# Kernel optimization log

Hardware: AMD Instinct MI355X
Metric: run time of the kernel (lower is better)

## Reference

```python
import jax, jax.numpy as jnp
import numpy as np

N = 512            # hidden_state
BATCH = 64
L = 8192           # seq_len; kernel_max_size == L so kernel length = L
MIN_DELTA = 1e-3
MAX_DELTA = 0.1


def _hippo(n):
    idx = np.arange(n)
    init = np.sqrt(2.0 * idx + 1.0)
    H = np.outer(init, init)           # init @ init.T
    H = np.tril(H)                      # zero strict upper triangle
    H[idx, idx] -= idx                  # diag -= arange(N)
    return (-H).astype(np.float32)


def setup_inputs() -> dict:
    key = jax.random.key(0)
    kx, kb, kc, kd = jax.random.split(key, 4)
    X = jax.random.normal(kx, (BATCH, L), dtype=jnp.float32)
    A = jnp.asarray(_hippo(N))                                   # [N,N] HiPPO init
    Bm = jax.random.normal(kb, (N, 1), dtype=jnp.float32) * (1.0 / N) ** 0.5
    C = jax.random.normal(kc, (1, N), dtype=jnp.float32)
    D = jnp.ones((1,), dtype=jnp.float32)
    log_delta = jax.random.uniform(
        kd, (1,), dtype=jnp.float32,
        minval=np.log(MIN_DELTA), maxval=np.log(MAX_DELTA))
    return {"X": X, "A": A, "Bm": Bm, "C": C, "D": D, "log_delta": log_delta}


def reference(X, A, Bm, C, D, log_delta):
    # delta = exp(clamp(log_delta, log(min), log(max)))
    delta = jnp.exp(jnp.clip(log_delta, jnp.log(MIN_DELTA), jnp.log(MAX_DELTA)))[0]
    # bilinear (Tustin) discretization
    I = jnp.eye(N, dtype=X.dtype)
    A1 = I - delta * 0.5 * A
    A2 = I + delta * 0.5 * A
    Ad = jnp.linalg.solve(A1, A2)           # [N,N]
    Bd = jnp.linalg.solve(A1, delta * Bm)   # [N,1]

    # kernel k[t] = C @ Ad^t @ Bd, t = 0..L-1 (sequential scan)
    def step(v, _):
        return Ad @ v, (C @ v)[0, 0]
    _, k = jax.lax.scan(step, Bd, None, length=L)  # [L]

    # FFT linear (causal) convolution, truncated to L
    end = L + L - 1
    Xd = jnp.fft.rfft(X, n=end, axis=-1)      # [B, F]
    Kd = jnp.fft.rfft(k, n=end)               # [F]
    y = jnp.fft.irfft(Xd * Kd, n=end, axis=-1)[..., :L]
    return y + D * X
```

## Files before the change

kernel.cpp:

```cpp
#include <hip/hip_runtime.h>

#define N 512
#define L 8192

#define LOG_MIN -6.907755278982137f
#define LOG_MAX -2.302585092994046f

typedef __attribute__((ext_vector_type(8))) short short8;
typedef __attribute__((ext_vector_type(4))) float f32x4;

__device__ __forceinline__ float get_delta(const float* logd) {
  float ld = logd[0];
  ld = fminf(fmaxf(ld, LOG_MIN), LOG_MAX);
  return expf(ld);
}
__device__ __forceinline__ unsigned short f2bf(float x) {
  union { float f; unsigned int u; } c; c.f = x;
  unsigned int u = c.u;
  u += 0x7FFFu + ((u >> 16) & 1u);
  return (unsigned short)(u >> 16);
}
__device__ __forceinline__ unsigned int pack2(unsigned short a, unsigned short b) {
  return (unsigned int)a | ((unsigned int)b << 16);
}

__device__ __forceinline__ void ast(float* p, float v) {
  __hip_atomic_store(p, v, __ATOMIC_RELAXED, __HIP_MEMORY_SCOPE_AGENT);
}
__device__ __forceinline__ void ast4(float* p, float4 v) {
  ast(p, v.x); ast(p + 1, v.y); ast(p + 2, v.z); ast(p + 3, v.w);
}
__device__ __forceinline__ void astu(unsigned* p, unsigned v) {
  __hip_atomic_store(p, v, __ATOMIC_RELAXED, __HIP_MEMORY_SCOPE_AGENT);
}

__device__ __forceinline__ void gsync(unsigned* bar, int p, unsigned tgt) {
  asm volatile("s_waitcnt vmcnt(0)" ::: "memory");
  __syncthreads();
  if (threadIdx.x == 0) {
    __hip_atomic_fetch_add(&bar[p], 1u, __ATOMIC_RELAXED, __HIP_MEMORY_SCOPE_AGENT);
    while (__hip_atomic_load(&bar[p], __ATOMIC_RELAXED, __HIP_MEMORY_SCOPE_AGENT) < tgt)
      __builtin_amdgcn_s_sleep(2);
  }
  __syncthreads();
}


__device__ void diag64(const float* __restrict__ A, float h,
                       float* __restrict__ Xi, int blk, int tid, float* sm) {
  float* Ash = sm;
  float* xs  = sm + 4160;
  float* dinv = sm + 8320;
  int i0 = blk * 64;
  int r = tid >> 2, c0 = (tid & 3) * 16;
#pragma unroll
  for (int q = 0; q < 16; q += 4) {
    float4 v = *(const float4*)(A + (size_t)(i0 + r) * N + i0 + c0 + q);
    Ash[r * 65 + c0 + q] = v.x; Ash[r * 65 + c0 + q + 1] = v.y;
    Ash[r * 65 + c0 + q + 2] = v.z; Ash[r * 65 + c0 + q + 3] = v.w;
  }
  for (int i = tid; i < 4160; i += 256) xs[i] = 0.f;
  __syncthreads();
  if (tid < 64) dinv[tid] = 1.f / (1.f - h * Ash[tid * 65 + tid]);
  __syncthreads();
  int t = tid >> 2, sub = tid & 3;
  for (int rr = 0; rr < 64; ++rr) {
    if (t <= rr) {
      float s = 0.f;
      for (int k = t + sub; k < rr; k += 4) s += Ash[rr * 65 + k] * xs[k * 65 + t];
      s += __shfl_xor(s, 1, 64);
      s += __shfl_xor(s, 2, 64);
      if (sub == 0)
        xs[rr * 65 + t] = (((rr == t) ? 1.f : 0.f) + h * s) * dinv[rr];
    }
  }
  __syncthreads();
#pragma unroll
  for (int q = 0; q < 16; q += 4) {
    float4 v = {xs[r * 65 + c0 + q], xs[r * 65 + c0 + q + 1],
                xs[r * 65 + c0 + q + 2], xs[r * 65 + c0 + q + 3]};
    ast4(Xi + (size_t)(i0 + r) * N + i0 + c0 + q, v);
  }
}

template <int NT>
__device__ void gemm32t(const float* __restrict__ A_, int lda,
                        const float* __restrict__ B_, int ldb,
                        float* __restrict__ C_, int ldc,
                        int bi, int bj, float alpha, int tid, float* sm) {
  float* As = sm;
  float* Bs = sm + 1056;
  int tx = tid & 31, ty = tid >> 5;
  int lr = tid >> 3, lc = (tid & 7) * 4;
  const float* ap = A_ + (size_t)(bi * 32 + lr) * lda + lc;
  const float* bp = B_ + (size_t)lr * ldb + bj * 32 + lc;
  float4 aR[NT], bR[NT];
#pragma unroll
  for (int t = 0; t < NT; ++t) {
    aR[t] = *(const float4*)(ap + 32 * t);
    bR[t] = *(const float4*)(bp + (size_t)(32 * t) * ldb);
  }
  float acc[4] = {0.f, 0.f, 0.f, 0.f};
#pragma unroll
  for (int t = 0; t < NT; ++t) {
    As[lr * 33 + lc] = aR[t].x; As[lr * 33 + lc + 1] = aR[t].y;
    As[lr * 33 + lc + 2] = aR[t].z; As[lr * 33 + lc + 3] = aR[t].w;
    Bs[lr * 33 + lc] = bR[t].x; Bs[lr * 33 + lc + 1] = bR[t].y;
    Bs[lr * 33 + lc + 2] = bR[t].z; Bs[lr * 33 + lc + 3] = bR[t].w;
    __syncthreads();
#pragma unroll
    for (int kk = 0; kk < 32; ++kk) {
      float bv = Bs[kk * 33 + tx];
#pragma unroll
      for (int m = 0; m < 4; ++m) acc[m] += As[(ty + 8 * m) * 33 + kk] * bv;
    }
    __syncthreads();
  }
#pragma unroll
  for (int m = 0; m < 4; ++m)
    ast(&C_[(size_t)(bi * 32 + ty + 8 * m) * ldc + bj * 32 + tx], alpha * acc[m]);
}

__device__ void sq32(const float* __restrict__ P, float* __restrict__ Q,
                     int bi, int bj, int first, int tid, float* sm) {
  float* As = sm;
  float* Bs = sm + 1056;
  int tx = tid & 31, ty = tid >> 5;
  int lr = tid >> 3, lc = (tid & 7) * 4;
  int nk = bi - bj + 1;
  int kb0 = bj * 32;
  int arow = bi * 32 + lr;
  const float* ap = P + (size_t)arow * N + lc;
  const float* bp = P + bj * 32 + lc;
  float4 aR[16], bR[16];
#pragma unroll
  for (int t = 0; t < 16; ++t) {
    if (t < nk) {
      int kt = kb0 + 32 * t;
      aR[t] = *(const float4*)(ap + kt);
      bR[t] = *(const float4*)(bp + (size_t)(kt + lr) * N);
    }
  }
  float acc[4] = {0.f, 0.f, 0.f, 0.f};
#pragma unroll
  for (int t = 0; t < 16; ++t) {
    if (t < nk) {
      int kb = kb0 + 32 * t;
      float a4[4] = {aR[t].x, aR[t].y, aR[t].z, aR[t].w};
      float b4[4] = {bR[t].x, bR[t].y, bR[t].z, bR[t].w};
      if (first) {
#pragma unroll
        for (int j = 0; j < 4; ++j) {
          a4[j] = 2.f * a4[j] - ((arow == kb + lc + j) ? 1.f : 0.f);
          b4[j] = 2.f * b4[j] - ((kb + lr == bj * 32 + lc + j) ? 1.f : 0.f);
        }
      }
      As[lr * 33 + lc] = a4[0]; As[lr * 33 + lc + 1] = a4[1];
      As[lr * 33 + lc + 2] = a4[2]; As[lr * 33 + lc + 3] = a4[3];
      Bs[lr * 33 + lc] = b4[0]; Bs[lr * 33 + lc + 1] = b4[1];
      Bs[lr * 33 + lc + 2] = b4[2]; Bs[lr * 33 + lc + 3] = b4[3];
      __syncthreads();
#pragma unroll
      for (int kk = 0; kk < 32; ++kk) {
        float bv = Bs[kk * 33 + tx];
#pragma unroll
        for (int m = 0; m < 4; ++m) acc[m] += As[(ty + 8 * m) * 33 + kk] * bv;
      }
      __syncthreads();
    }
  }
#pragma unroll
  for (int m = 0; m < 4; ++m)
    ast(&Q[(size_t)(bi * 32 + ty + 8 * m) * N + bj * 32 + tx], acc[m]);
}

__device__ void vstep_g(const float* __restrict__ P, float* __restrict__ Vtr,
                        int base, int first, int idx, int tid, float* sm) {
  int bi = idx & 15, cj = idx >> 4;
  float* As = sm;
  float* Bs = sm + 1056;
  int tx = tid & 31, ty = tid >> 5;
  int lr = tid >> 3, lc = (tid & 7) * 4;
  int nrow = bi * 32 + lr;
  int crow = cj * 32 + lr;
  int cok = (crow < base);
  const float* ap = P + (size_t)nrow * N + lc;
  const float* bp = Vtr + (size_t)crow * N + lc;
  int nk = bi + 1;
  float4 aR[16], bR[16];
#pragma unroll
  for (int t = 0; t < 16; ++t) {
    if (t < nk) {
      aR[t] = *(const float4*)(ap + 32 * t);
      bR[t] = cok ? *(const float4*)(bp + 32 * t) : make_float4(0.f, 0.f, 0.f, 0.f);
    }
  }
  float acc[4] = {0.f, 0.f, 0.f, 0.f};
#pragma unroll
  for (int t = 0; t < 16; ++t) {
    if (t < nk) {
      int kb = 32 * t;
      float a4[4] = {aR[t].x, aR[t].y, aR[t].z, aR[t].w};
      if (first) {
#pragma unroll
        for (int j = 0; j < 4; ++j)
          a4[j] = 2.f * a4[j] - ((nrow == kb + lc + j) ? 1.f : 0.f);
      }
      As[lr * 33 + lc] = a4[0]; As[lr * 33 + lc + 1] = a4[1];
      As[lr * 33 + lc + 2] = a4[2]; As[lr * 33 + lc + 3] = a4[3];
      Bs[lr * 33 + lc] = bR[t].x; Bs[lr * 33 + lc + 1] = bR[t].y;
      Bs[lr * 33 + lc + 2] = bR[t].z; Bs[lr * 33 + lc + 3] = bR[t].w;
      __syncthreads();
#pragma unroll
      for (int kk = 0; kk < 32; ++kk) {
        float bv = Bs[tx * 33 + kk];
#pragma unroll
        for (int m = 0; m < 4; ++m) acc[m] += As[(ty + 8 * m) * 33 + kk] * bv;
      }
      __syncthreads();
    }
  }
  int c = cj * 32 + tx;
  if (c < base) {
#pragma unroll
    for (int m = 0; m < 4; ++m)
      ast(&Vtr[(size_t)(base + c) * N + bi * 32 + ty + 8 * m], acc[m]);
  }
}

__device__ void wstep_g(const float* __restrict__ P, float* __restrict__ W,
                        int base, int cj, int tid, float* sm) {
  float* As = sm;
  float* Bs = sm + 1056;
  int tx = tid & 31, ty = tid >> 5;
  int lr = tid >> 3, lc = (tid & 7) * 4;
  int qok = (lr < base);
  const float* ap = W + (size_t)lr * N + lc;
  const float* bp = P + cj * 32 + lc;
  int kb0 = cj * 32;
  int nk = 16 - cj;
  float4 aR[16], bR[16];
#pragma unroll
  for (int t = 0; t < 16; ++t) {
    if (t < nk) {
      int kt = kb0 + 32 * t;
      aR[t] = qok ? *(const float4*)(ap + kt) : make_float4(0.f, 0.f, 0.f, 0.f);
      bR[t] = *(const float4*)(bp + (size_t)(kt + lr) * N);
    }
  }
  float acc[4] = {0.f, 0.f, 0.f, 0.f};
#pragma unroll
  for (int t = 0; t < 16; ++t) {
    if (t < nk) {
      As[lr * 33 + lc] = aR[t].x; As[lr * 33 + lc + 1] = aR[t].y;
      As[lr * 33 + lc + 2] = aR[t].z; As[lr * 33 + lc + 3] = aR[t].w;
      Bs[lr * 33 + lc] = bR[t].x; Bs[lr * 33 + lc + 1] = bR[t].y;
      Bs[lr * 33 + lc + 2] = bR[t].z; Bs[lr * 33 + lc + 3] = bR[t].w;
      __syncthreads();
#pragma unroll
      for (int kk = 0; kk < 32; ++kk) {
        float bv = Bs[kk * 33 + tx];
#pragma unroll
        for (int m = 0; m < 4; ++m) acc[m] += As[(ty + 8 * m) * 33 + kk] * bv;
      }
      __syncthreads();
    }
  }
#pragma unroll
  for (int m = 0; m < 4; ++m) {
    int q = ty + 8 * m;
    if (q < base) ast(&W[(size_t)(base + q) * N + cj * 32 + tx], acc[m]);
  }
}

__device__ void kfinal_g(const float* __restrict__ W, const float* __restrict__ Vtr,
                         float* __restrict__ kvec, int bi, int bj, int tid, float* sm) {
  float* As = sm;
  float* Bs = sm + 1056;
  int tx = tid & 31, ty = tid >> 5;
  int lr = tid >> 3, lc = (tid & 7) * 4;
  const float* ap = W + (size_t)(bi * 32 + lr) * N + lc;
  const float* bp = Vtr + (size_t)(bj * 32 + lr) * N + lc;
  float4 aR[16], bR[16];
#pragma unroll
  for (int t = 0; t < 16; ++t) {
    aR[t] = *(const float4*)(ap + 32 * t);
    bR[t] = *(const float4*)(bp + 32 * t);
  }
  float acc[4] = {0.f, 0.f, 0.f, 0.f};
#pragma unroll
  for (int t = 0; t < 16; ++t) {
    As[lr * 33 + lc] = aR[t].x; As[lr * 33 + lc + 1] = aR[t].y;
    As[lr * 33 + lc + 2] = aR[t].z; As[lr * 33 + lc + 3] = aR[t].w;
    Bs[lr * 33 + lc] = bR[t].x; Bs[lr * 33 + lc + 1] = bR[t].y;
    Bs[lr * 33 + lc + 2] = bR[t].z; Bs[lr * 33 + lc + 3] = bR[t].w;
    __syncthreads();
#pragma unroll
    for (int kk = 0; kk < 32; ++kk) {
      float bv = Bs[tx * 33 + kk];
#pragma unroll
      for (int m = 0; m < 4; ++m) acc[m] += As[(ty + 8 * m) * 33 + kk] * bv;
    }
    __syncthreads();
  }
#pragma unroll
  for (int m = 0; m < 4; ++m)
    ast(&kvec[(size_t)(bi * 32 + ty + 8 * m) * 128 + bj * 32 + tx], acc[m]);
}

__device__ void bd1_body(const float* __restrict__ Xi, const float* __restrict__ Bm,
                         float delta, float* __restrict__ Vtr, int blk, int tid,
                         float* sm) {
  float* bs = sm;
  if (tid < 128) ((float4*)bs)[tid] = ((const float4*)Bm)[tid];
  __syncthreads();
  int w = tid >> 6, lane = tid & 63;
#pragma unroll
  for (int pass = 0; pass < 2; ++pass) {
    int row = blk * 8 + w * 2 + pass;
    const float* Xr = Xi + (size_t)row * N + lane * 8;
    float4 a0 = *(const float4*)Xr;
    float4 a1 = *(const float4*)(Xr + 4);
    const float* bp = bs + lane * 8;
    float acc = a0.x * bp[0] + a0.y * bp[1] + a0.z * bp[2] + a0.w * bp[3]
              + a1.x * bp[4] + a1.y * bp[5] + a1.z * bp[6] + a1.w * bp[7];
    acc += __shfl_xor(acc, 1, 64);
    acc += __shfl_xor(acc, 2, 64);
    acc += __shfl_xor(acc, 4, 64);
    acc += __shfl_xor(acc, 8, 64);
    acc += __shfl_xor(acc, 16, 64);
    acc += __shfl_xor(acc, 32, 64);
    if (lane == 0) ast(&Vtr[row], delta * acc);
  }
}

__device__ __forceinline__ void afrag_unit(const float* __restrict__ X,
                                           unsigned* __restrict__ Atab, int u) {
  int lane = u & 63;
  int f = u >> 6;
  int bt = f >> 8, ut = f & 255;
  int row = bt * 16 + (lane & 15);
  int u0 = ut * 32 + ((lane >> 4) << 3);
  const float* xp = X + (size_t)row * L + u0;
  unsigned short v[8];
#pragma unroll
  for (int e = 0; e < 8; ++e) v[e] = f2bf(xp[e]);
  unsigned* q = Atab + ((size_t)f * 64 + lane) * 4;
  astu(q, pack2(v[0], v[1])); astu(q + 1, pack2(v[2], v[3]));
  astu(q + 2, pack2(v[4], v[5])); astu(q + 3, pack2(v[6], v[7]));
}

__device__ __forceinline__ void bfrag_unit(const float* __restrict__ kvec,
                                           unsigned* __restrict__ Btab, int u) {
  int lane = u & 63;
  int si = u >> 6;
  int base = si * 16 + (lane & 15) - ((lane >> 4) << 3);
  unsigned short v[8];
#pragma unroll
  for (int e = 0; e < 8; ++e) {
    int idx = base - e;
    float x = (idx >= 0) ? kvec[idx] : 0.0f;
    v[e] = f2bf(x);
  }
  unsigned* q = Btab + ((size_t)si * 64 + lane) * 4;
  astu(q, pack2(v[0], v[1])); astu(q + 1, pack2(v[2], v[3]));
  astu(q + 2, pack2(v[4], v[5])); astu(q + 3, pack2(v[6], v[7]));
}

#define NB 168u

__global__ __launch_bounds__(256, 2) void k_chain(
    const float* __restrict__ A, const float* __restrict__ Bm,
    const float* __restrict__ C, const float* __restrict__ logd,
    const float* __restrict__ X,
    float* __restrict__ Xi, float* __restrict__ U1, float* __restrict__ U2,
    float* __restrict__ U3, float* __restrict__ PB,
    float* __restrict__ Vtr, float* __restrict__ W, float* __restrict__ kvec,
    unsigned* __restrict__ Atab, unsigned* __restrict__ Btab,
    unsigned* bar) {
  __shared__ float sm[8704];
  int b = blockIdx.x, tid = threadIdx.x;
  float delta = get_delta(logd);
  float h = 0.5f * delta;
#define PBUF(i) (PB + (size_t)(i) * (N * N))

  int sbi = 0, srem = b;
  while (srem > sbi) { srem -= (sbi + 1); ++sbi; }
  int sbj = srem;

  if (b < 8) {
    diag64(A, h, Xi, b, tid, sm);
  } else if (b < 36) {
    int idx = b - 8, bi = 0, bj = 0, cnt = 0;
    for (int i = 0; i < 8; ++i)
      for (int j = i + 1; j < 8; ++j) { if (cnt == idx) { bi = i; bj = j; } ++cnt; }
    int r = tid >> 2, c0 = (tid & 3) * 16;
    float4 z = {0.f, 0.f, 0.f, 0.f};
#pragma unroll
    for (int q = 0; q < 16; q += 4)
      ast4(Xi + (size_t)(bi * 64 + r) * N + bj * 64 + c0 + q, z);
  } else if (b == 36) {
    for (int i = tid; i < N; i += 256) ast(&W[i], C[i]);
  } else if (b >= 40) {
    int base = (b - 40) * 512;
    afrag_unit(X, Atab, base + tid);
    afrag_unit(X, Atab, base + 256 + tid);
  }
  gsync(bar, 0, NB);
  if (b < 16) {
    int g = b >> 2, t = b & 3;
    gemm32t<2>(A + (size_t)(128 * g + 64) * N + 128 * g, N,
               Xi + (size_t)(128 * g) * (N + 1), N,
               U1 + g * 4096, 64, t >> 1, t & 1, 1.0f, tid, sm);
  }
  gsync(bar, 1, NB);
  if (b < 16) {
    int g = b >> 2, t = b & 3;
    gemm32t<2>(Xi + (size_t)(128 * g + 64) * (N + 1), N, U1 + g * 4096, 64,
               Xi + (size_t)(128 * g + 64) * N + 128 * g, N, t >> 1, t & 1, h, tid, sm);
  }
  gsync(bar, 2, NB);
  if (b < 32) {
    int g = b >> 4, t = b & 15;
    gemm32t<4>(A + (size_t)(256 * g + 128) * N + 256 * g, N,
               Xi + (size_t)(256 * g) * (N + 1), N,
               U2 + g * 16384, 128, t >> 2, t & 3, 1.0f, tid, sm);
  }
  gsync(bar, 3, NB);
  if (b < 32) {
    int g = b >> 4, t = b & 15;
    gemm32t<4>(Xi + (size_t)(256 * g + 128) * (N + 1), N, U2 + g * 16384, 128,
               Xi + (size_t)(256 * g + 128) * N + 256 * g, N, t >> 2, t & 3, h, tid, sm);
  }
  gsync(bar, 4, NB);
  if (b < 64)
    gemm32t<8>(A + (size_t)256 * N, N, Xi, N, U3, 256, b >> 3, b & 7, 1.0f, tid, sm);
  gsync(bar, 5, NB);
  if (b < 64)
    gemm32t<8>(Xi + (size_t)256 * (N + 1), N, U3, 256,
               Xi + (size_t)256 * N, N, b >> 3, b & 7, h, tid, sm);
  gsync(bar, 6, NB);
  if (b < 64) bd1_body(Xi, Bm, delta, Vtr, b, tid, sm);
  gsync(bar, 7, NB);
  if (b < 136) sq32(Xi, PBUF(0), sbi, sbj, 1, tid, sm);
  else if (b < 152) vstep_g(Xi, Vtr, 1, 1, b - 136, tid, sm);
  gsync(bar, 8, NB);
  if (b < 136) sq32(PBUF(0), PBUF(1), sbi, sbj, 0, tid, sm);
  else if (b < 152) vstep_g(PBUF(0), Vtr, 2, 0, b - 136, tid, sm);
  gsync(bar, 9, NB);
  if (b < 136) sq32(PBUF(1), PBUF(2), sbi, sbj, 0, tid, sm);
  else if (b < 152) vstep_g(PBUF(1), Vtr, 4, 0, b - 136, tid, sm);
  gsync(bar, 10, NB);
  if (b < 136) sq32(PBUF(2), PBUF(3), sbi, sbj, 0, tid, sm);
  else if (b < 152) vstep_g(PBUF(2), Vtr, 8, 0, b - 136, tid, sm);
  gsync(bar, 11, NB);
  if (b < 136) sq32(PBUF(3), PBUF(4), sbi, sbj, 0, tid, sm);
  else if (b < 152) vstep_g(PBUF(3), Vtr, 16, 0, b - 136, tid, sm);
  gsync(bar, 12, NB);
  if (b < 136) sq32(PBUF(4), PBUF(5), sbi, sbj, 0, tid, sm);
  else if (b < 152) vstep_g(PBUF(4), Vtr, 32, 0, b - 136, tid, sm);
  gsync(bar, 13, NB);
  if (b < 136) sq32(PBUF(5), PBUF(6), sbi, sbj, 0, tid, sm);
  else vstep_g(PBUF(5), Vtr, 64, 0, b - 136, tid, sm);
  gsync(bar, 14, NB);
  if (b < 136) sq32(PBUF(6), PBUF(7), sbi, sbj, 0, tid, sm);
  else if (b < 152) wstep_g(PBUF(6), W, 1, b - 136, tid, sm);
  gsync(bar, 15, NB);
  if (b < 136) sq32(PBUF(7), PBUF(8), sbi, sbj, 0, tid, sm);
  else if (b < 152) wstep_g(PBUF(7), W, 2, b - 136, tid, sm);
  gsync(bar, 16, NB);
  if (b < 136) sq32(PBUF(8), PBUF(9), sbi, sbj, 0, tid, sm);
  else if (b < 152) wstep_g(PBUF(8), W, 4, b - 136, tid, sm);
  gsync(bar, 17, NB);
  if (b < 136) sq32(PBUF(9), PBUF(10), sbi, sbj, 0, tid, sm);
  else if (b < 152) wstep_g(PBUF(9), W, 8, b - 136, tid, sm);
  gsync(bar, 18, NB);
  if (b < 136) sq32(PBUF(10), PBUF(11), sbi, sbj, 0, tid, sm);
  else if (b < 152) wstep_g(PBUF(10), W, 16, b - 136, tid, sm);
  gsync(bar, 19, NB);
  if (b >= 136 && b < 152) wstep_g(PBUF(11), W, 32, b - 136, tid, sm);
  gsync(bar, 20, NB);
  if (b < 8) kfinal_g(W, Vtr, kvec, b >> 2, b & 3, tid, sm);
  gsync(bar, 21, NB);
  if (b < 128) bfrag_unit(kvec, Btab, b * 256 + tid);
#undef PBUF
}

__global__ __launch_bounds__(256, 2) void k_convmm(const short8* __restrict__ Atab,
                                                   const short8* __restrict__ Btab,
                                                   const float* __restrict__ X,
                                                   const float* __restrict__ Dp,
                                                   float* __restrict__ Y) {
  __shared__ short8 bsh[32][64];
  int tid = threadIdx.x, lane = tid & 63, bt = tid >> 6;
  int p = blockIdx.x;
  int jL = p, jH = 511 - p;
  int nL = (jL + 2) >> 1, nH = (jH + 2) >> 1;
  f32x4 aL = {0.f, 0.f, 0.f, 0.f}, aH = {0.f, 0.f, 0.f, 0.f};
  const short8* Abase = Atab + (size_t)bt * 256 * 64 + lane;
  for (int u0 = 0; u0 < nH; u0 += 16) {
#pragma unroll
    for (int k = 0; k < 8; ++k) {
      int idx = tid + 256 * k;
      int f = idx >> 6, ln = idx & 63;
      int i = f & 15;
      int ut = u0 + i;
      if (f < 16) {
        if (ut < nH) bsh[i][ln] = Btab[(size_t)(jH - 2 * ut) * 64 + ln];
      } else {
        if (ut < nL) bsh[16 + i][ln] = Btab[(size_t)(jL - 2 * ut) * 64 + ln];
      }
    }
    __syncthreads();
    int m = (nH - u0 < 16) ? (nH - u0) : 16;
    short8 a = Abase[(size_t)u0 * 64];
    for (int i = 0; i < m; ++i) {
      short8 an;
      if (i + 1 < m) an = Abase[(size_t)(u0 + i + 1) * 64];
      aH = __builtin_amdgcn_mfma_f32_16x16x32_bf16(a, bsh[i][lane], aH, 0, 0, 0);
      if (u0 + i < nL)
        aL = __builtin_amdgcn_mfma_f32_16x16x32_bf16(a, bsh[16 + i][lane], aL, 0, 0, 0);
      a = an;
    }
    __syncthreads();
  }
  float D0 = Dp[0];
  int tt = lane & 15, rq = (lane >> 4) << 2;
#pragma unroll
  for (int r = 0; r < 4; ++r) {
    int bb = bt * 16 + rq + r;
    size_t oL = (size_t)bb * L + jL * 16 + tt;
    size_t oH = (size_t)bb * L + jH * 16 + tt;
    Y[oL] = aL[r] + D0 * X[oL];
    Y[oH] = aH[r] + D0 * X[oH];
  }
}

extern "C" void kernel_launch(void* const* d_in, const int* in_sizes, int n_in,
                              void* d_out, int out_size, void* d_ws, size_t ws_size,
                              hipStream_t stream) {
  const float* X  = (const float*)d_in[0];
  const float* A  = (const float*)d_in[1];
  const float* Bm = (const float*)d_in[2];
  const float* C  = (const float*)d_in[3];
  const float* D  = (const float*)d_in[4];
  const float* ld = (const float*)d_in[5];
  float* Y = (float*)d_out;

  float* ws = (float*)d_ws;
  unsigned* bar = (unsigned*)ws;
  float* kv  = ws + 64;
  float* Vtr = ws + 8256;
  float* W   = ws + 73792;
  float* Xi  = ws + 106560;
  float* U1  = ws + 368704;
  float* U2  = ws + 385088;
  float* U3  = ws + 417856;
  float* PB  = ws + 483392;
  unsigned* Atab = (unsigned*)(ws + 3629120);
  unsigned* Btab = (unsigned*)(ws + 3891264);

  hipMemsetAsync(bar, 0, 64 * sizeof(unsigned), stream);
  k_chain<<<168, 256, 0, stream>>>(A, Bm, C, ld, X, Xi, U1, U2, U3, PB, Vtr, W, kv,
                                   Atab, Btab, bar);
  k_convmm<<<256, 256, 0, stream>>>((const short8*)Atab, (const short8*)Btab, X, D, Y);
}
```

Before: 505.7 us.

## Cut grid-barrier count and switch to leader-broadcast barrier in chain kernel

The chain kernel's grid barrier changes so only block 0 spins on the arrival counter and then publishes a go flag that the other blocks poll. The first inverse level's two dependent GEMMs are fused into one per-block routine, removing a barrier and the U1 buffer. The Bd computation is overlapped with the first squaring step, and vstep now loops over column tiles so 16 blocks cover it. The grid shrinks from 168 to 152 blocks. The net effect is fewer global synchronization points, at the cost of more serial work per block in some phases.

Result: slower. 601.7 us (+19.0%).

```diff
diff --git a/kernel.cpp b/kernel.cpp
--- a/kernel.cpp
+++ b/kernel.cpp
@@ -34,13 +34,21 @@
   __hip_atomic_store(p, v, __ATOMIC_RELAXED, __HIP_MEMORY_SCOPE_AGENT);
 }
 
-__device__ __forceinline__ void gsync(unsigned* bar, int p, unsigned tgt) {
+#define NB 152u
+
+__device__ __forceinline__ void gsync(unsigned* bar, unsigned* go, int p, int isb0) {
   asm volatile("s_waitcnt vmcnt(0)" ::: "memory");
   __syncthreads();
   if (threadIdx.x == 0) {
     __hip_atomic_fetch_add(&bar[p], 1u, __ATOMIC_RELAXED, __HIP_MEMORY_SCOPE_AGENT);
-    while (__hip_atomic_load(&bar[p], __ATOMIC_RELAXED, __HIP_MEMORY_SCOPE_AGENT) < tgt)
-      __builtin_amdgcn_s_sleep(2);
+    if (isb0) {
+      while (__hip_atomic_load(&bar[p], __ATOMIC_RELAXED, __HIP_MEMORY_SCOPE_AGENT) < NB)
+        __builtin_amdgcn_s_sleep(4);
+      __hip_atomic_store(&go[p], 1u, __ATOMIC_RELAXED, __HIP_MEMORY_SCOPE_AGENT);
+    } else {
+      while (__hip_atomic_load(&go[p], __ATOMIC_RELAXED, __HIP_MEMORY_SCOPE_AGENT) == 0u)
+        __builtin_amdgcn_s_sleep(4);
+    }
   }
   __syncthreads();
 }
@@ -81,6 +89,71 @@
                 xs[r * 65 + c0 + q + 2], xs[r * 65 + c0 + q + 3]};
     ast4(Xi + (size_t)(i0 + r) * N + i0 + c0 + q, v);
   }
+}
+
+__device__ void lvl64_fused(const float* __restrict__ A, float* __restrict__ Xi,
+                            float h, int g, int tid, float* sm) {
+  float* X11s = sm;
+  float* Us   = sm + 4160;
+  int b11 = 128 * g, b22 = 128 * g + 64;
+  int r = tid >> 2, c0 = (tid & 3) * 16;
+#pragma unroll
+  for (int q = 0; q < 16; q += 4) {
+    float4 v = *(const float4*)(Xi + (size_t)(b11 + r) * N + b11 + c0 + q);
+    X11s[r * 65 + c0 + q] = v.x; X11s[r * 65 + c0 + q + 1] = v.y;
+    X11s[r * 65 + c0 + q + 2] = v.z; X11s[r * 65 + c0 + q + 3] = v.w;
+  }
+  float4 aR[16];
+#pragma unroll
+  for (int t = 0; t < 16; ++t)
+    aR[t] = *(const float4*)(A + (size_t)(b22 + r) * N + b11 + 4 * t);
+  __syncthreads();
+  float u[16];
+#pragma unroll
+  for (int j = 0; j < 16; ++j) u[j] = 0.f;
+#pragma unroll 4
+  for (int k4 = 0; k4 < 16; ++k4) {
+    float av[4] = {aR[k4].x, aR[k4].y, aR[k4].z, aR[k4].w};
+#pragma unroll
+    for (int s = 0; s < 4; ++s) {
+      int k = 4 * k4 + s;
+      float aa = av[s];
+#pragma unroll
+      for (int j = 0; j < 16; j += 4) {
+        float4 xv = *(const float4*)&X11s[k * 65 + c0 + j];
+        u[j] += aa * xv.x; u[j + 1] += aa * xv.y;
+        u[j + 2] += aa * xv.z; u[j + 3] += aa * xv.w;
+      }
+    }
+  }
+  float4 xR[16];
+#pragma unroll
+  for (int t = 0; t < 16; ++t)
+    xR[t] = *(const float4*)(Xi + (size_t)(b22 + r) * N + b22 + 4 * t);
+#pragma unroll
+  for (int j = 0; j < 16; ++j) Us[r * 65 + c0 + j] = u[j];
+  __syncthreads();
+  float x[16];
+#pragma unroll
+  for (int j = 0; j < 16; ++j) x[j] = 0.f;
+#pragma unroll 4
+  for (int k4 = 0; k4 < 16; ++k4) {
+    float av[4] = {xR[k4].x, xR[k4].y, xR[k4].z, xR[k4].w};
+#pragma unroll
+    for (int s = 0; s < 4; ++s) {
+      int k = 4 * k4 + s;
+      float aa = av[s];
+#pragma unroll
+      for (int j = 0; j < 16; j += 4) {
+        float4 xv = *(const float4*)&Us[k * 65 + c0 + j];
+        x[j] += aa * xv.x; x[j + 1] += aa * xv.y;
+        x[j + 2] += aa * xv.z; x[j + 3] += aa * xv.w;
+      }
+    }
+  }
+#pragma unroll
+  for (int j = 0; j < 16; ++j)
+    ast(&Xi[(size_t)(b22 + r) * N + b11 + c0 + j], h * x[j]);
 }
 
 template <int NT>
@@ -175,56 +248,60 @@
 }
 
 __device__ void vstep_g(const float* __restrict__ P, float* __restrict__ Vtr,
-                        int base, int first, int idx, int tid, float* sm) {
-  int bi = idx & 15, cj = idx >> 4;
+                        int base, int first, int bi, int tid, float* sm) {
   float* As = sm;
   float* Bs = sm + 1056;
   int tx = tid & 31, ty = tid >> 5;
   int lr = tid >> 3, lc = (tid & 7) * 4;
   int nrow = bi * 32 + lr;
-  int crow = cj * 32 + lr;
-  int cok = (crow < base);
   const float* ap = P + (size_t)nrow * N + lc;
-  const float* bp = Vtr + (size_t)crow * N + lc;
   int nk = bi + 1;
-  float4 aR[16], bR[16];
-#pragma unroll
-  for (int t = 0; t < 16; ++t) {
-    if (t < nk) {
-      aR[t] = *(const float4*)(ap + 32 * t);
-      bR[t] = cok ? *(const float4*)(bp + 32 * t) : make_float4(0.f, 0.f, 0.f, 0.f);
-    }
-  }
-  float acc[4] = {0.f, 0.f, 0.f, 0.f};
-#pragma unroll
-  for (int t = 0; t < 16; ++t) {
-    if (t < nk) {
-      int kb = 32 * t;
-      float a4[4] = {aR[t].x, aR[t].y, aR[t].z, aR[t].w};
-      if (first) {
-#pragma unroll
-        for (int j = 0; j < 4; ++j)
-          a4[j] = 2.f * a4[j] - ((nrow == kb + lc + j) ? 1.f : 0.f);
+  float4 aR[16];
+#pragma unroll
+  for (int t = 0; t < 16; ++t)
+    if (t < nk) aR[t] = *(const float4*)(ap + 32 * t);
+  int ncj = (base > 32) ? 2 : 1;
+  for (int cj = 0; cj < ncj; ++cj) {
+    int crow = cj * 32 + lr;
+    int cok = (crow < base);
+    const float* bp = Vtr + (size_t)crow * N + lc;
+    float4 bR[16];
+#pragma unroll
+    for (int t = 0; t < 16; ++t)
+      if (t < nk) bR[t] = cok ? *(const float4*)(bp + 32 * t)
+                              : make_float4(0.f, 0.f, 0.f, 0.f);
+    float acc[4] = {0.f, 0.f, 0.f, 0.f};
+#pragma unroll
+    for (int t = 0; t < 16; ++t) {
+      if (t < nk) {
+        int kb = 32 * t;
+        float a4[4] = {aR[t].x, aR[t].y, aR[t].z, aR[t].w};
+        if (first) {
+#pragma unroll
+          for (int j = 0; j < 4; ++j)
+            a4[j] = 2.f * a4[j] - ((nrow == kb + lc + j) ? 1.f : 0.f);
+        }
+        As[lr * 33 + lc] = a4[0]; As[lr * 33 + lc + 1] = a4[1];
+        As[lr * 33 + lc + 2] = a4[2]; As[lr * 33 + lc + 3] = a4[3];
+        Bs[lr * 33 + lc] = bR[t].x; Bs[lr * 33 + lc + 1] = bR[t].y;
+        Bs[lr * 33 + lc + 2] = bR[t].z; Bs[lr * 33 + lc + 3] = bR[t].w;
+        __syncthreads();
+#pragma unroll
+        for (int kk = 0; kk < 32; ++kk) {
+          float bv = Bs[tx * 33 + kk];
+#pragma unroll
+          for (int m = 0; m < 4; ++m) acc[m] += As[(ty + 8 * m) * 33 + kk] * bv;
+        }
+        __syncthreads();
       }
-      As[lr * 33 + lc] = a4[0]; As[lr * 33 + lc + 1] = a4[1];
-      As[lr * 33 + lc + 2] = a4[2]; As[lr * 33 + lc + 3] = a4[3];
-      Bs[lr * 33 + lc] = bR[t].x; Bs[lr * 33 + lc + 1] = bR[t].y;
-      Bs[lr * 33 + lc + 2] = bR[t].z; Bs[lr * 33 + lc + 3] = bR[t].w;
-      __syncthreads();
-#pragma unroll
-      for (int kk = 0; kk < 32; ++kk) {
-        float bv = Bs[tx * 33 + kk];
-#pragma unroll
-        for (int m = 0; m < 4; ++m) acc[m] += As[(ty + 8 * m) * 33 + kk] * bv;
-      }
-      __syncthreads();
-    }
-  }
-  int c = cj * 32 + tx;
-  if (c < base) {
-#pragma unroll
-    for (int m = 0; m < 4; ++m)
-      ast(&Vtr[(size_t)(base + c) * N + bi * 32 + ty + 8 * m], acc[m]);
+    }
+    int c = cj * 32 + tx;
+    if (c < base) {
+#pragma unroll
+      for (int m = 0; m < 4; ++m)
+        ast(&Vtr[(size_t)(base + c) * N + bi * 32 + ty + 8 * m], acc[m]);
+    }
+    if (ncj == 2 && cj == 0) __syncthreads();
   }
 }
 
@@ -309,15 +386,15 @@
 }
 
 __device__ void bd1_body(const float* __restrict__ Xi, const float* __restrict__ Bm,
-                         float delta, float* __restrict__ Vtr, int blk, int tid,
+                         float delta, float* __restrict__ Vtr, int bb, int tid,
                          float* sm) {
   float* bs = sm;
   if (tid < 128) ((float4*)bs)[tid] = ((const float4*)Bm)[tid];
   __syncthreads();
   int w = tid >> 6, lane = tid & 63;
 #pragma unroll
-  for (int pass = 0; pass < 2; ++pass) {
-    int row = blk * 8 + w * 2 + pass;
+  for (int pass = 0; pass < 8; ++pass) {
+    int row = bb * 32 + w * 8 + pass;
     const float* Xr = Xi + (size_t)row * N + lane * 8;
     float4 a0 = *(const float4*)Xr;
     float4 a1 = *(const float4*)(Xr + 4);
@@ -367,22 +444,23 @@
   astu(q + 2, pack2(v[4], v[5])); astu(q + 3, pack2(v[6], v[7]));
 }
 
-#define NB 168u
-
-__global__ __launch_bounds__(256, 2) void k_chain(
+__global__ __launch_bounds__(256) void k_chain(
     const float* __restrict__ A, const float* __restrict__ Bm,
     const float* __restrict__ C, const float* __restrict__ logd,
     const float* __restrict__ X,
-    float* __restrict__ Xi, float* __restrict__ U1, float* __restrict__ U2,
-    float* __restrict__ U3, float* __restrict__ PB,
+    float* __restrict__ Xi, float* __restrict__ U2, float* __restrict__ U3,
+    float* __restrict__ PB,
     float* __restrict__ Vtr, float* __restrict__ W, float* __restrict__ kvec,
     unsigned* __restrict__ Atab, unsigned* __restrict__ Btab,
     unsigned* bar) {
   __shared__ float sm[8704];
   int b = blockIdx.x, tid = threadIdx.x;
+  int isb0 = (b == 0);
+  unsigned* go = bar + 32;
   float delta = get_delta(logd);
   float h = 0.5f * delta;
 #define PBUF(i) (PB + (size_t)(i) * (N * N))
+#define GS(p) gsync(bar, go, (p), isb0)
 
   int sbi = 0, srem = b;
   while (srem > sbi) { srem -= (sbi + 1); ++sbi; }
@@ -401,88 +479,77 @@
       ast4(Xi + (size_t)(bi * 64 + r) * N + bj * 64 + c0 + q, z);
   } else if (b == 36) {
     for (int i = tid; i < N; i += 256) ast(&W[i], C[i]);
-  } else if (b >= 40) {
-    int base = (b - 40) * 512;
-    afrag_unit(X, Atab, base + tid);
-    afrag_unit(X, Atab, base + 256 + tid);
-  }
-  gsync(bar, 0, NB);
-  if (b < 16) {
-    int g = b >> 2, t = b & 3;
-    gemm32t<2>(A + (size_t)(128 * g + 64) * N + 128 * g, N,
-               Xi + (size_t)(128 * g) * (N + 1), N,
-               U1 + g * 4096, 64, t >> 1, t & 1, 1.0f, tid, sm);
-  }
-  gsync(bar, 1, NB);
-  if (b < 16) {
-    int g = b >> 2, t = b & 3;
-    gemm32t<2>(Xi + (size_t)(128 * g + 64) * (N + 1), N, U1 + g * 4096, 64,
-               Xi + (size_t)(128 * g + 64) * N + 128 * g, N, t >> 1, t & 1, h, tid, sm);
-  }
-  gsync(bar, 2, NB);
+  } else {
+    for (int u = (b - 37) * 256 + tid; u < 65536; u += 115 * 256)
+      afrag_unit(X, Atab, u);
+  }
+  GS(0);
+  if (b < 4) lvl64_fused(A, Xi, h, b, tid, sm);
+  GS(1);
   if (b < 32) {
     int g = b >> 4, t = b & 15;
     gemm32t<4>(A + (size_t)(256 * g + 128) * N + 256 * g, N,
                Xi + (size_t)(256 * g) * (N + 1), N,
                U2 + g * 16384, 128, t >> 2, t & 3, 1.0f, tid, sm);
   }
-  gsync(bar, 3, NB);
+  GS(2);
   if (b < 32) {
     int g = b >> 4, t = b & 15;
     gemm32t<4>(Xi + (size_t)(256 * g + 128) * (N + 1), N, U2 + g * 16384, 128,
                Xi + (size_t)(256 * g + 128) * N + 256 * g, N, t >> 2, t & 3, h, tid, sm);
   }
-  gsync(bar, 4, NB);
+  GS(3);
   if (b < 64)
     gemm32t<8>(A + (size_t)256 * N, N, Xi, N, U3, 256, b >> 3, b & 7, 1.0f, tid, sm);
-  gsync(bar, 5, NB);
+  GS(4);
   if (b < 64)
     gemm32t<8>(Xi + (size_t)256 * (N + 1), N, U3, 256,
                Xi + (size_t)256 * N, N, b >> 3, b & 7, h, tid, sm);
-  gsync(bar, 6, NB);
-  if (b < 64) bd1_body(Xi, Bm, delta, Vtr, b, tid, sm);
-  gsync(bar, 7, NB);
+  GS(5);
   if (b < 136) sq32(Xi, PBUF(0), sbi, sbj, 1, tid, sm);
-  else if (b < 152) vstep_g(Xi, Vtr, 1, 1, b - 136, tid, sm);
-  gsync(bar, 8, NB);
+  else bd1_body(Xi, Bm, delta, Vtr, b - 136, tid, sm);
+  GS(6);
   if (b < 136) sq32(PBUF(0), PBUF(1), sbi, sbj, 0, tid, sm);
-  else if (b < 152) vstep_g(PBUF(0), Vtr, 2, 0, b - 136, tid, sm);
-  gsync(bar, 9, NB);
+  else vstep_g(Xi, Vtr, 1, 1, b - 136, tid, sm);
+  GS(7);
   if (b < 136) sq32(PBUF(1), PBUF(2), sbi, sbj, 0, tid, sm);
-  else if (b < 152) vstep_g(PBUF(1), Vtr, 4, 0, b - 136, tid, sm);
-  gsync(bar, 10, NB);
+  else vstep_g(PBUF(0), Vtr, 2, 0, b - 136, tid, sm);
+  GS(8);
   if (b < 136) sq32(PBUF(2), PBUF(3), sbi, sbj, 0, tid, sm);
-  else if (b < 152) vstep_g(PBUF(2), Vtr, 8, 0, b - 136, tid, sm);
-  gsync(bar, 11, NB);
+  else vstep_g(PBUF(1), Vtr, 4, 0, b - 136, tid, sm);
+  GS(9);
   if (b < 136) sq32(PBUF(3), PBUF(4), sbi, sbj, 0, tid, sm);
-  else if (b < 152) vstep_g(PBUF(3), Vtr, 16, 0, b - 136, tid, sm);
-  gsync(bar, 12, NB);
+  else vstep_g(PBUF(2), Vtr, 8, 0, b - 136, tid, sm);
+  GS(10);
   if (b < 136) sq32(PBUF(4), PBUF(5), sbi, sbj, 0, tid, sm);
-  else if (b < 152) vstep_g(PBUF(4), Vtr, 32, 0, b - 136, tid, sm);
-  gsync(bar, 13, NB);
+  else vstep_g(PBUF(3), Vtr, 16, 0, b - 136, tid, sm);
+  GS(11);
   if (b < 136) sq32(PBUF(5), PBUF(6), sbi, sbj, 0, tid, sm);
+  else vstep_g(PBUF(4), Vtr, 32, 0, b - 136, tid, sm);
+  GS(12);
+  if (b < 136) sq32(PBUF(6), PBUF(7), sbi, sbj, 0, tid, sm);
   else vstep_g(PBUF(5), Vtr, 64, 0, b - 136, tid, sm);
-  gsync(bar, 14, NB);
-  if (b < 136) sq32(PBUF(6), PBUF(7), sbi, sbj, 0, tid, sm);
-  else if (b < 152) wstep_g(PBUF(6), W, 1, b - 136, tid, sm);
-  gsync(bar, 15, NB);
+  GS(13);
   if (b < 136) sq32(PBUF(7), PBUF(8), sbi, sbj, 0, tid, sm);
-  else if (b < 152) wstep_g(PBUF(7), W, 2, b - 136, tid, sm);
-  gsync(bar, 16, NB);
+  else wstep_g(PBUF(6), W, 1, b - 136, tid, sm);
+  GS(14);
   if (b < 136) sq32(PBUF(8), PBUF(9), sbi, sbj, 0, tid, sm);
-  else if (b < 152) wstep_g(PBUF(8), W, 4, b - 136, tid, sm);
-  gsync(bar, 17, NB);
+  else wstep_g(PBUF(7), W, 2, b - 136, tid, sm);
+  GS(15);
   if (b < 136) sq32(PBUF(9), PBUF(10), sbi, sbj, 0, tid, sm);
-  else if (b < 152) wstep_g(PBUF(9), W, 8, b - 136, tid, sm);
-  gsync(bar, 18, NB);
+  else wstep_g(PBUF(8), W, 4, b - 136, tid, sm);
+  GS(16);
   if (b < 136) sq32(PBUF(10), PBUF(11), sbi, sbj, 0, tid, sm);
-  else if (b < 152) wstep_g(PBUF(10), W, 16, b - 136, tid, sm);
-  gsync(bar, 19, NB);
-  if (b >= 136 && b < 152) wstep_g(PBUF(11), W, 32, b - 136, tid, sm);
-  gsync(bar, 20, NB);
+  else wstep_g(PBUF(9), W, 8, b - 136, tid, sm);
+  GS(17);
+  if (b < 16) wstep_g(PBUF(10), W, 16, b, tid, sm);
+  GS(18);
+  if (b < 16) wstep_g(PBUF(11), W, 32, b, tid, sm);
+  GS(19);
   if (b < 8) kfinal_g(W, Vtr, kvec, b >> 2, b & 3, tid, sm);
-  gsync(bar, 21, NB);
+  GS(20);
   if (b < 128) bfrag_unit(kvec, Btab, b * 256 + tid);
+#undef GS
 #undef PBUF
 }
 
@@ -553,7 +620,6 @@
   float* Vtr = ws + 8256;
   float* W   = ws + 73792;
   float* Xi  = ws + 106560;
-  float* U1  = ws + 368704;
   float* U2  = ws + 385088;
   float* U3  = ws + 417856;
   float* PB  = ws + 483392;
@@ -561,7 +627,7 @@
   unsigned* Btab = (unsigned*)(ws + 3891264);
 
   hipMemsetAsync(bar, 0, 64 * sizeof(unsigned), stream);
-  k_chain<<<168, 256, 0, stream>>>(A, Bm, C, ld, X, Xi, U1, U2, U3, PB, Vtr, W, kv,
+  k_chain<<<152, 256, 0, stream>>>(A, Bm, C, ld, X, Xi, U2, U3, PB, Vtr, W, kv,
                                    Atab, Btab, bar);
   k_convmm<<<256, 256, 0, stream>>>((const short8*)Atab, (const short8*)Btab, X, D, Y);
 }
```
